# Optimization experiments

Hardware: AMD Instinct MI355X
Metric: run time of the kernel (lower is better)

## Reference

```python
import jax, jax.numpy as jnp
import numpy as np

N_NODES = 100000
N_EDGES = 1600000
IN_DIM = 64
OUT_DIM = 64
BN_EPS = 1e-5


def batchnorm(h, gamma, beta):
    # BatchNorm1d in training mode: per-feature batch stats, biased variance
    mean = jnp.mean(h, axis=0)
    var = jnp.mean((h - mean) ** 2, axis=0)
    return gamma * (h - mean) * jax.lax.rsqrt(var + BN_EPS) + beta


def setup_inputs() -> dict:
    key = jax.random.key(0)
    ks = jax.random.split(key, 4)
    x = jax.random.normal(ks[0], (N_NODES, IN_DIM), dtype=jnp.float32)
    edge_index = jax.random.randint(ks[1], (2, N_EDGES), 0, N_NODES, dtype=jnp.int32)
    epsilon = jnp.asarray(0.1, dtype=jnp.float32)
    # Linear weights stored [in, out] (transpose of torch layout)
    W1 = jax.random.normal(ks[2], (IN_DIM, 2 * OUT_DIM), dtype=jnp.float32) * (1.0 / np.sqrt(IN_DIM))
    b1 = jnp.zeros((2 * OUT_DIM,), dtype=jnp.float32)
    g1 = jnp.ones((2 * OUT_DIM,), dtype=jnp.float32)
    be1 = jnp.zeros((2 * OUT_DIM,), dtype=jnp.float32)
    W2 = jax.random.normal(ks[3], (2 * OUT_DIM, OUT_DIM), dtype=jnp.float32) * (1.0 / np.sqrt(2 * OUT_DIM))
    b2 = jnp.zeros((OUT_DIM,), dtype=jnp.float32)
    g2 = jnp.ones((OUT_DIM,), dtype=jnp.float32)
    be2 = jnp.zeros((OUT_DIM,), dtype=jnp.float32)
    return {"x": x, "edge_index": edge_index, "epsilon": epsilon,
            "W1": W1, "b1": b1, "g1": g1, "be1": be1,
            "W2": W2, "b2": b2, "g2": g2, "be2": be2}


def reference(x, edge_index, epsilon, W1, b1, g1, be1, W2, b2, g2, be2):
    src, dst = edge_index[0], edge_index[1]
    # gather messages from src, scatter-add into dst  [N, D]
    neighbor_sum = jnp.zeros_like(x).at[dst].add(x[src])
    combined = (1.0 + epsilon) * x + neighbor_sum
    h = combined @ W1 + b1            # [N, 2*out_dim]
    h = jax.nn.relu(batchnorm(h, g1, be1))
    h = h @ W2 + b2                   # [N, out_dim]
    return batchnorm(h, g2, be2)
```

## Files before the change

kernel.cpp:

```cpp
#include <hip/hip_runtime.h>

#define N_NODES 100000
#define N_EDGES 1600000
#define IN_DIM 64
#define H_DIM 128
#define OUT_DIM 64
#define BN_EPS 1e-5f
#define CAP 64
#define BIN_SHIFT 9
#define BIN_NODES 512
#define NB 256
#define NBIN_BLOCKS ((N_NODES + BIN_NODES - 1) / BIN_NODES)

#define OFF_XB     0
#define OFF_BINNED 3200000
#define OFF_COMB   3200000
#define OFF_SRCL   6400000
#define OFF_H1     6400000
#define OFF_H2     12800000
#define OFF_CNT    16000000
#define OFF_STATS  19200000
#define S1SUM 0
#define S1SQ  128
#define S2SUM 256
#define S2SQ  320

#define DEV_ATOMIC_ADD(p, v) __hip_atomic_fetch_add((p), (v), __ATOMIC_RELAXED, __HIP_MEMORY_SCOPE_AGENT)

typedef __attribute__((ext_vector_type(8))) short short8;
typedef __attribute__((ext_vector_type(4))) float f32x4;

__device__ __forceinline__ unsigned short f2bf(float f) {
  union { float f; unsigned u; } v; v.f = f;
  unsigned r = v.u + 0x7FFFu + ((v.u >> 16) & 1u);
  return (unsigned short)(r >> 16);
}
__device__ __forceinline__ float bflo(unsigned v) { union { unsigned u; float f; } t; t.u = v << 16; return t.f; }
__device__ __forceinline__ float bfhi(unsigned v) { union { unsigned u; float f; } t; t.u = v & 0xFFFF0000u; return t.f; }

__device__ __forceinline__ void acc8(float* a, uint4 v) {
  a[0] += bflo(v.x); a[1] += bfhi(v.x); a[2] += bflo(v.y); a[3] += bfhi(v.y);
  a[4] += bflo(v.z); a[5] += bfhi(v.z); a[6] += bflo(v.w); a[7] += bfhi(v.w);
}
__device__ __forceinline__ uint4 pack8(const float* a) {
  uint4 o;
  o.x = (unsigned)f2bf(a[0]) | ((unsigned)f2bf(a[1]) << 16);
  o.y = (unsigned)f2bf(a[2]) | ((unsigned)f2bf(a[3]) << 16);
  o.z = (unsigned)f2bf(a[4]) | ((unsigned)f2bf(a[5]) << 16);
  o.w = (unsigned)f2bf(a[6]) | ((unsigned)f2bf(a[7]) << 16);
  return o;
}

__global__ __launch_bounds__(256) void k_prep(const float* __restrict__ x,
                                              unsigned short* __restrict__ xb,
                                              const int* __restrict__ ei,
                                              int* __restrict__ bhist) {
  __shared__ int h[NB];
  const int tid = threadIdx.x;
  h[tid] = 0;
  #pragma unroll
  for (int j = 0; j < 8; ++j) {
    int i = blockIdx.x * 2048 + j * 256 + tid;
    if (i < N_NODES * IN_DIM / 4) {
      float4 v = ((const float4*)x)[i];
      ushort4 o;
      o.x = f2bf(v.x); o.y = f2bf(v.y); o.z = f2bf(v.z); o.w = f2bf(v.w);
      *(ushort4*)(xb + i * 4) = o;
    }
  }
  __syncthreads();
  #pragma unroll
  for (int j = 0; j < 8; ++j) {
    int e = blockIdx.x * 2048 + j * 256 + tid;
    if (e < N_EDGES) atomicAdd(&h[ei[N_EDGES + e] >> BIN_SHIFT], 1);
  }
  __syncthreads();
  if (h[tid]) DEV_ATOMIC_ADD(&bhist[tid], h[tid]);
}

__global__ __launch_bounds__(256) void k_scan256(const int* __restrict__ bhist,
                                                 int* __restrict__ boff,
                                                 int* __restrict__ bcur) {
  __shared__ int s[NB];
  const int tid = threadIdx.x;
  int v = bhist[tid];
  s[tid] = v;
  __syncthreads();
  for (int d = 1; d < NB; d <<= 1) {
    int t = (tid >= d) ? s[tid - d] : 0;
    __syncthreads();
    s[tid] += t;
    __syncthreads();
  }
  int incl = s[tid];
  boff[tid] = incl - v;
  if (tid == NB - 1) boff[NB] = incl;
  bcur[tid] = incl - v;
}

__global__ __launch_bounds__(256) void k_bsplit(const int* __restrict__ ei,
                                                int* __restrict__ bcur,
                                                int2* __restrict__ binned) {
  __shared__ int lcnt[NB];
  __shared__ int lofs[NB];
  __shared__ int lbase[NB];
  __shared__ int sc[NB];
  __shared__ int2 staged[2048];
  const int tid = threadIdx.x;
  lcnt[tid] = 0;
  __syncthreads();
  int src[8], dst[8], rk[8];
  #pragma unroll
  for (int j = 0; j < 8; ++j) {
    int e = blockIdx.x * 2048 + j * 256 + tid;
    if (e < N_EDGES) {
      src[j] = ei[e];
      dst[j] = ei[N_EDGES + e];
      rk[j] = atomicAdd(&lcnt[dst[j] >> BIN_SHIFT], 1);
    } else {
      src[j] = -1;
    }
  }
  __syncthreads();
  int v = lcnt[tid];
  sc[tid] = v;
  __syncthreads();
  for (int d = 1; d < NB; d <<= 1) {
    int t = (tid >= d) ? sc[tid - d] : 0;
    __syncthreads();
    sc[tid] += t;
    __syncthreads();
  }
  lofs[tid] = sc[tid] - v;
  if (v > 0) lbase[tid] = DEV_ATOMIC_ADD(&bcur[tid], v);
  __syncthreads();
  #pragma unroll
  for (int j = 0; j < 8; ++j) {
    if (src[j] >= 0) {
      int b = dst[j] >> BIN_SHIFT;
      staged[lofs[b] + rk[j]] = make_int2(src[j], dst[j]);
    }
  }
  int nv = sc[NB - 1];
  __syncthreads();
  for (int i = tid; i < nv; i += 256) {
    int2 e = staged[i];
    int b = e.y >> BIN_SHIFT;
    binned[lbase[b] + (i - lofs[b])] = e;
  }
}

__global__ __launch_bounds__(512) void k_bfill(const int* __restrict__ boff,
                                               const int2* __restrict__ binned,
                                               int* __restrict__ cnt,
                                               int* __restrict__ srcl) {
  __shared__ int lcnt[BIN_NODES];
  const int tid = threadIdx.x;
  for (int i = tid; i < BIN_NODES; i += 512) lcnt[i] = 0;
  __syncthreads();
  const int b = blockIdx.x;
  const int s = boff[b], e = boff[b + 1];
  const int base = b * BIN_NODES;
  for (int i = s + tid; i < e; i += 512) {
    int2 ed = binned[i];
    int pos = atomicAdd(&lcnt[ed.y - base], 1);
    if (pos < CAP) srcl[ed.y * CAP + pos] = ed.x;
  }
  __syncthreads();
  for (int i = tid; i < BIN_NODES; i += 512) {
    int node = base + i;
    if (node < N_NODES) cnt[node] = lcnt[i];
  }
}

__global__ __launch_bounds__(256, 5) void k_gather(const unsigned short* __restrict__ xb,
                                                   const float* __restrict__ eps,
                                                   const int* __restrict__ cnt,
                                                   const int* __restrict__ srcl,
                                                   unsigned short* __restrict__ comb) {
  const int t = blockIdx.x * 256 + threadIdx.x;
  const int node = t >> 3;
  const int sub = t & 7;
  if (node >= N_NODES) return;

  float a[8];
  {
    uint4 sv = *(const uint4*)(xb + node * 64 + sub * 8);
    float e1 = 1.0f + eps[0];
    a[0] = bflo(sv.x) * e1; a[1] = bfhi(sv.x) * e1;
    a[2] = bflo(sv.y) * e1; a[3] = bfhi(sv.y) * e1;
    a[4] = bflo(sv.z) * e1; a[5] = bfhi(sv.z) * e1;
    a[6] = bflo(sv.w) * e1; a[7] = bfhi(sv.w) * e1;
  }
  int deg = cnt[node];
  if (deg > CAP) deg = CAP;
  const int* sl = srcl + node * CAP;

  uint4 n0 = *(const uint4*)sl;
  uint4 n1 = *(const uint4*)(sl + 4);
  int j = 0;
  while (j + 8 <= deg) {
    uint4 i0 = n0, i1 = n1;
    uint4 r0 = *(const uint4*)(xb + (size_t)i0.x * 64 + sub * 8);
    uint4 r1 = *(const uint4*)(xb + (size_t)i0.y * 64 + sub * 8);
    uint4 r2 = *(const uint4*)(xb + (size_t)i0.z * 64 + sub * 8);
    uint4 r3 = *(const uint4*)(xb + (size_t)i0.w * 64 + sub * 8);
    uint4 r4 = *(const uint4*)(xb + (size_t)i1.x * 64 + sub * 8);
    uint4 r5 = *(const uint4*)(xb + (size_t)i1.y * 64 + sub * 8);
    uint4 r6 = *(const uint4*)(xb + (size_t)i1.z * 64 + sub * 8);
    uint4 r7 = *(const uint4*)(xb + (size_t)i1.w * 64 + sub * 8);
    j += 8;
    n0 = *(const uint4*)(sl + j);
    n1 = *(const uint4*)(sl + j + 4);
    acc8(a, r0); acc8(a, r1); acc8(a, r2); acc8(a, r3);
    acc8(a, r4); acc8(a, r5); acc8(a, r6); acc8(a, r7);
  }
  if (j + 4 <= deg) {
    uint4 i0 = *(const uint4*)(sl + j);
    uint4 r0 = *(const uint4*)(xb + (size_t)i0.x * 64 + sub * 8);
    uint4 r1 = *(const uint4*)(xb + (size_t)i0.y * 64 + sub * 8);
    uint4 r2 = *(const uint4*)(xb + (size_t)i0.z * 64 + sub * 8);
    uint4 r3 = *(const uint4*)(xb + (size_t)i0.w * 64 + sub * 8);
    acc8(a, r0); acc8(a, r1); acc8(a, r2); acc8(a, r3);
    j += 4;
  }
  if (j + 2 <= deg) {
    int2 i2 = *(const int2*)(sl + j);
    uint4 r0 = *(const uint4*)(xb + (size_t)i2.x * 64 + sub * 8);
    uint4 r1 = *(const uint4*)(xb + (size_t)i2.y * 64 + sub * 8);
    acc8(a, r0); acc8(a, r1);
    j += 2;
  }
  if (j < deg) {
    int s0 = sl[j];
    uint4 r0 = *(const uint4*)(xb + (size_t)s0 * 64 + sub * 8);
    acc8(a, r0);
  }
  *(uint4*)(comb + node * 64 + sub * 8) = pack8(a);
}

#define APAD 72
__global__ __launch_bounds__(256) void k_gemm1(const unsigned short* __restrict__ comb,
                                               const float* __restrict__ W1,
                                               const float* __restrict__ b1,
                                               unsigned short* __restrict__ h1,
                                               float* __restrict__ stats) {
  __shared__ unsigned short As[128 * APAD];
  __shared__ unsigned short Ws[128 * APAD];
  __shared__ float red[4][128];
  const int tid = threadIdx.x;
  const int wv = tid >> 6, lane = tid & 63;
  const int quad = lane >> 4, ln = lane & 15;
  const int rowBase = blockIdx.x * 128;

  #pragma unroll
  for (int it = 0; it < 8; ++it) {
    int idx = it * 256 + tid;
    int k = idx >> 5, n4 = idx & 31;
    float4 wv1 = *(const float4*)(W1 + k * 128 + n4 * 4);
    Ws[(n4 * 4 + 0) * APAD + k] = f2bf(wv1.x);
    Ws[(n4 * 4 + 1) * APAD + k] = f2bf(wv1.y);
    Ws[(n4 * 4 + 2) * APAD + k] = f2bf(wv1.z);
    Ws[(n4 * 4 + 3) * APAD + k] = f2bf(wv1.w);
  }
  #pragma unroll
  for (int it = 0; it < 4; ++it) {
    int idx = it * 256 + tid;
    int row = idx >> 3, ch = idx & 7;
    int g = rowBase * 8 + idx;
    uint4 u = (g < N_NODES * 8) ? ((const uint4*)comb)[g] : make_uint4(0, 0, 0, 0);
    *(uint4*)&As[row * APAD + ch * 8] = u;
  }
  __syncthreads();

  f32x4 acc[2][8];
  #pragma unroll
  for (int mt = 0; mt < 2; ++mt) {
    #pragma unroll
    for (int nt = 0; nt < 8; ++nt) acc[mt][nt] = (f32x4)0.0f;
  }
  const int rw = wv * 32;
  #pragma unroll
  for (int kb = 0; kb < 2; ++kb) {
    short8 a0 = *(short8*)&As[(rw + ln) * APAD + kb * 32 + quad * 8];
    short8 a1 = *(short8*)&As[(rw + 16 + ln) * APAD + kb * 32 + quad * 8];
    #pragma unroll
    for (int nt = 0; nt < 8; ++nt) {
      short8 b = *(short8*)&Ws[(nt * 16 + ln) * APAD + kb * 32 + quad * 8];
      acc[0][nt] = __builtin_amdgcn_mfma_f32_16x16x32_bf16(a0, b, acc[0][nt], 0, 0, 0);
      acc[1][nt] = __builtin_amdgcn_mfma_f32_16x16x32_bf16(a1, b, acc[1][nt], 0, 0, 0);
    }
  }

  float bias[8], s[8], q[8];
  #pragma unroll
  for (int nt = 0; nt < 8; ++nt) { bias[nt] = b1[nt * 16 + ln]; s[nt] = 0.f; q[nt] = 0.f; }
  #pragma unroll
  for (int mt = 0; mt < 2; ++mt) {
    #pragma unroll
    for (int i = 0; i < 4; ++i) {
      int gRow = rowBase + rw + mt * 16 + quad * 4 + i;
      if (gRow < N_NODES) {
        #pragma unroll
        for (int nt = 0; nt < 8; ++nt) {
          float v = acc[mt][nt][i] + bias[nt];
          h1[gRow * 128 + nt * 16 + ln] = f2bf(v);
          s[nt] += v; q[nt] += v * v;
        }
      }
    }
  }
  #pragma unroll
  for (int nt = 0; nt < 8; ++nt) {
    s[nt] += __shfl_xor(s[nt], 16); s[nt] += __shfl_xor(s[nt], 32);
    q[nt] += __shfl_xor(q[nt], 16); q[nt] += __shfl_xor(q[nt], 32);
  }
  if (lane < 16) {
    #pragma unroll
    for (int nt = 0; nt < 8; ++nt) red[wv][nt * 16 + ln] = s[nt];
  }
  __syncthreads();
  if (tid < 128) DEV_ATOMIC_ADD(&stats[S1SUM + tid],
                                red[0][tid] + red[1][tid] + red[2][tid] + red[3][tid]);
  __syncthreads();
  if (lane < 16) {
    #pragma unroll
    for (int nt = 0; nt < 8; ++nt) red[wv][nt * 16 + ln] = q[nt];
  }
  __syncthreads();
  if (tid < 128) DEV_ATOMIC_ADD(&stats[S1SQ + tid],
                                red[0][tid] + red[1][tid] + red[2][tid] + red[3][tid]);
}

#define WPAD 136
__global__ __launch_bounds__(256) void k_gemm2(const unsigned short* __restrict__ h1,
                                               const float* __restrict__ W2,
                                               const float* __restrict__ b2,
                                               const float* __restrict__ g1,
                                               const float* __restrict__ be1,
                                               unsigned short* __restrict__ h2,
                                               float* __restrict__ stats) {
  __shared__ unsigned short As[128 * APAD];
  __shared__ unsigned short Ws[64 * WPAD];
  __shared__ float red[4][64];
  __shared__ float scL[128], shL[128];
  const int tid = threadIdx.x;
  const int wv = tid >> 6, lane = tid & 63;
  const int quad = lane >> 4, ln = lane & 15;
  const int rowBase = blockIdx.x * 128;

  if (tid < 128) {
    float mean = stats[S1SUM + tid] * (1.0f / N_NODES);
    float var = stats[S1SQ + tid] * (1.0f / N_NODES) - mean * mean;
    var = fmaxf(var, 0.0f);
    float sc = g1[tid] * rsqrtf(var + BN_EPS);
    scL[tid] = sc;
    shL[tid] = be1[tid] - mean * sc;
  }
  #pragma unroll
  for (int it = 0; it < 8; ++it) {
    int idx = it * 256 + tid;
    int k = idx >> 4, n4 = idx & 15;
    float4 wv2 = *(const float4*)(W2 + k * 64 + n4 * 4);
    Ws[(n4 * 4 + 0) * WPAD + k] = f2bf(wv2.x);
    Ws[(n4 * 4 + 1) * WPAD + k] = f2bf(wv2.y);
    Ws[(n4 * 4 + 2) * WPAD + k] = f2bf(wv2.z);
    Ws[(n4 * 4 + 3) * WPAD + k] = f2bf(wv2.w);
  }

  f32x4 acc[2][4];
  #pragma unroll
  for (int mt = 0; mt < 2; ++mt) {
    #pragma unroll
    for (int nt = 0; nt < 4; ++nt) acc[mt][nt] = (f32x4)0.0f;
  }
  const int rw = wv * 32;

  for (int kc = 0; kc < 2; ++kc) {
    __syncthreads();
    #pragma unroll
    for (int it = 0; it < 4; ++it) {
      int idx = it * 256 + tid;
      int row = idx >> 3, ch = idx & 7;
      int gRow = rowBase + row;
      uint4 u = (gRow < N_NODES) ? *(const uint4*)(h1 + gRow * 128 + kc * 64 + ch * 8)
                                 : make_uint4(0, 0, 0, 0);
      int kb = kc * 64 + ch * 8;
      float f0 = fmaxf(bflo(u.x) * scL[kb + 0] + shL[kb + 0], 0.f);
      float f1 = fmaxf(bfhi(u.x) * scL[kb + 1] + shL[kb + 1], 0.f);
      float f2 = fmaxf(bflo(u.y) * scL[kb + 2] + shL[kb + 2], 0.f);
      float f3 = fmaxf(bfhi(u.y) * scL[kb + 3] + shL[kb + 3], 0.f);
      float f4 = fmaxf(bflo(u.z) * scL[kb + 4] + shL[kb + 4], 0.f);
      float f5 = fmaxf(bfhi(u.z) * scL[kb + 5] + shL[kb + 5], 0.f);
      float f6 = fmaxf(bflo(u.w) * scL[kb + 6] + shL[kb + 6], 0.f);
      float f7 = fmaxf(bfhi(u.w) * scL[kb + 7] + shL[kb + 7], 0.f);
      uint4 o;
      o.x = (unsigned)f2bf(f0) | ((unsigned)f2bf(f1) << 16);
      o.y = (unsigned)f2bf(f2) | ((unsigned)f2bf(f3) << 16);
      o.z = (unsigned)f2bf(f4) | ((unsigned)f2bf(f5) << 16);
      o.w = (unsigned)f2bf(f6) | ((unsigned)f2bf(f7) << 16);
      *(uint4*)&As[row * APAD + ch * 8] = o;
    }
    __syncthreads();
    #pragma unroll
    for (int kb = 0; kb < 2; ++kb) {
      short8 a0 = *(short8*)&As[(rw + ln) * APAD + kb * 32 + quad * 8];
      short8 a1 = *(short8*)&As[(rw + 16 + ln) * APAD + kb * 32 + quad * 8];
      #pragma unroll
      for (int nt = 0; nt < 4; ++nt) {
        short8 b = *(short8*)&Ws[(nt * 16 + ln) * WPAD + kc * 64 + kb * 32 + quad * 8];
        acc[0][nt] = __builtin_amdgcn_mfma_f32_16x16x32_bf16(a0, b, acc[0][nt], 0, 0, 0);
        acc[1][nt] = __builtin_amdgcn_mfma_f32_16x16x32_bf16(a1, b, acc[1][nt], 0, 0, 0);
      }
    }
  }

  float bias[4], s[4], q[4];
  #pragma unroll
  for (int nt = 0; nt < 4; ++nt) { bias[nt] = b2[nt * 16 + ln]; s[nt] = 0.f; q[nt] = 0.f; }
  #pragma unroll
  for (int mt = 0; mt < 2; ++mt) {
    #pragma unroll
    for (int i = 0; i < 4; ++i) {
      int gRow = rowBase + rw + mt * 16 + quad * 4 + i;
      if (gRow < N_NODES) {
        #pragma unroll
        for (int nt = 0; nt < 4; ++nt) {
          float v = acc[mt][nt][i] + bias[nt];
          h2[gRow * 64 + nt * 16 + ln] = f2bf(v);
          s[nt] += v; q[nt] += v * v;
        }
      }
    }
  }
  #pragma unroll
  for (int nt = 0; nt < 4; ++nt) {
    s[nt] += __shfl_xor(s[nt], 16); s[nt] += __shfl_xor(s[nt], 32);
    q[nt] += __shfl_xor(q[nt], 16); q[nt] += __shfl_xor(q[nt], 32);
  }
  if (lane < 16) {
    #pragma unroll
    for (int nt = 0; nt < 4; ++nt) red[wv][nt * 16 + ln] = s[nt];
  }
  __syncthreads();
  if (tid < 64) DEV_ATOMIC_ADD(&stats[S2SUM + tid],
                               red[0][tid] + red[1][tid] + red[2][tid] + red[3][tid]);
  __syncthreads();
  if (lane < 16) {
    #pragma unroll
    for (int nt = 0; nt < 4; ++nt) red[wv][nt * 16 + ln] = q[nt];
  }
  __syncthreads();
  if (tid < 64) DEV_ATOMIC_ADD(&stats[S2SQ + tid],
                               red[0][tid] + red[1][tid] + red[2][tid] + red[3][tid]);
}

__global__ __launch_bounds__(256) void k_out(const unsigned short* __restrict__ h2,
                                             const float* __restrict__ stats,
                                             const float* __restrict__ g2,
                                             const float* __restrict__ be2,
                                             float* __restrict__ out) {
  __shared__ float scL[64], shL[64];
  const int tid = threadIdx.x;
  if (tid < 64) {
    float mean = stats[S2SUM + tid] * (1.0f / N_NODES);
    float var = stats[S2SQ + tid] * (1.0f / N_NODES) - mean * mean;
    var = fmaxf(var, 0.0f);
    float sc = g2[tid] * rsqrtf(var + BN_EPS);
    scL[tid] = sc;
    shL[tid] = be2[tid] - mean * sc;
  }
  __syncthreads();
  int i = blockIdx.x * 256 + tid;
  if (i < N_NODES * OUT_DIM / 4) {
    int c = i & 15;
    uint2 u = *(const uint2*)(h2 + i * 4);
    float4 v = {bflo(u.x), bfhi(u.x), bflo(u.y), bfhi(u.y)};
    float4 sc = ((const float4*)scL)[c];
    float4 sh = ((const float4*)shL)[c];
    v.x = v.x * sc.x + sh.x;
    v.y = v.y * sc.y + sh.y;
    v.z = v.z * sc.z + sh.z;
    v.w = v.w * sc.w + sh.w;
    ((float4*)out)[i] = v;
  }
}

extern "C" void kernel_launch(void* const* d_in, const int* in_sizes, int n_in,
                              void* d_out, int out_size, void* d_ws, size_t ws_size,
                              hipStream_t stream) {
  const float* x   = (const float*)d_in[0];
  const int*   ei  = (const int*)d_in[1];
  const float* eps = (const float*)d_in[2];
  const float* W1  = (const float*)d_in[3];
  const float* b1  = (const float*)d_in[4];
  const float* g1  = (const float*)d_in[5];
  const float* be1 = (const float*)d_in[6];
  const float* W2  = (const float*)d_in[7];
  const float* b2  = (const float*)d_in[8];
  const float* g2  = (const float*)d_in[9];
  const float* be2 = (const float*)d_in[10];

  float* ws = (float*)d_ws;
  unsigned short* xb     = (unsigned short*)(ws + OFF_XB);
  int2*           binned = (int2*)(ws + OFF_BINNED);
  unsigned short* comb   = (unsigned short*)(ws + OFF_COMB);
  int*            srcl   = (int*)(ws + OFF_SRCL);
  unsigned short* h1     = (unsigned short*)(ws + OFF_H1);
  unsigned short* h2     = (unsigned short*)(ws + OFF_H2);
  int*            cnt    = (int*)(ws + OFF_CNT);
  float*          stats  = ws + OFF_STATS;
  int*            bhist  = (int*)(stats + 768);
  int*            boff   = (int*)(stats + 1024);
  int*            bcur   = (int*)(stats + 1288);
  float*          out    = (float*)d_out;

  hipMemsetAsync(stats, 0, 1024 * sizeof(float), stream);

  const int edgeGrid = (N_EDGES + 2047) / 2048;
  const int gemmGrid = (N_NODES + 127) / 128;
  const int gatherGrid = (N_NODES * 8 + 255) / 256;
  k_prep<<<edgeGrid, 256, 0, stream>>>(x, xb, ei, bhist);
  k_scan256<<<1, NB, 0, stream>>>(bhist, boff, bcur);
  k_bsplit<<<edgeGrid, 256, 0, stream>>>(ei, bcur, binned);
  k_bfill<<<NBIN_BLOCKS, 512, 0, stream>>>(boff, binned, cnt, srcl);
  k_gather<<<gatherGrid, 256, 0, stream>>>(xb, eps, cnt, srcl, comb);
  k_gemm1<<<gemmGrid, 256, 0, stream>>>(comb, W1, b1, h1, stats);
  k_gemm2<<<gemmGrid, 256, 0, stream>>>(h1, W2, b2, g1, be1, h2, stats);
  k_out<<<(N_NODES * OUT_DIM / 4 + 255) / 256, 256, 0, stream>>>(h2, stats, g2, be2, out);
}
```

Baseline: 257.8 us.

## Fuse both GEMMs, batchnorms and output into one kernel with grid barriers

```diff
diff --git a/kernel.cpp b/kernel.cpp
--- a/kernel.cpp
+++ b/kernel.cpp
@@ -11,13 +11,12 @@
 #define BIN_NODES 512
 #define NB 256
 #define NBIN_BLOCKS ((N_NODES + BIN_NODES - 1) / BIN_NODES)
+#define MLP_GRID ((N_NODES + 127) / 128)
 
 #define OFF_XB     0
 #define OFF_BINNED 3200000
 #define OFF_COMB   3200000
 #define OFF_SRCL   6400000
-#define OFF_H1     6400000
-#define OFF_H2     12800000
 #define OFF_CNT    16000000
 #define OFF_STATS  19200000
 #define S1SUM 0
@@ -239,29 +238,53 @@
   *(uint4*)(comb + node * 64 + sub * 8) = pack8(a);
 }
 
-#define APAD 72
-__global__ __launch_bounds__(256) void k_gemm1(const unsigned short* __restrict__ comb,
-                                               const float* __restrict__ W1,
-                                               const float* __restrict__ b1,
-                                               unsigned short* __restrict__ h1,
-                                               float* __restrict__ stats) {
-  __shared__ unsigned short As[128 * APAD];
-  __shared__ unsigned short Ws[128 * APAD];
+#define KP 68
+#define HP 136
+
+__device__ __forceinline__ void gridbar(int* bar, int nblk) {
+  __syncthreads();
+  if (threadIdx.x == 0) {
+    __hip_atomic_fetch_add(bar, 1, __ATOMIC_ACQ_REL, __HIP_MEMORY_SCOPE_AGENT);
+    while (__hip_atomic_load(bar, __ATOMIC_ACQUIRE, __HIP_MEMORY_SCOPE_AGENT) < nblk) {
+      __builtin_amdgcn_s_sleep(4);
+    }
+  }
+  __syncthreads();
+}
+
+__global__ __launch_bounds__(256, 4) void k_mlp(const unsigned short* __restrict__ comb,
+                                                const float* __restrict__ W1,
+                                                const float* __restrict__ b1,
+                                                const float* __restrict__ g1,
+                                                const float* __restrict__ be1,
+                                                const float* __restrict__ W2,
+                                                const float* __restrict__ b2,
+                                                const float* __restrict__ g2,
+                                                const float* __restrict__ be2,
+                                                float* __restrict__ stats,
+                                                int* __restrict__ bar,
+                                                float* __restrict__ out) {
+  __shared__ unsigned short smem[17408];
   __shared__ float red[4][128];
+  __shared__ float scl[128], shl[128];
+  unsigned short* As  = smem;
+  unsigned short* Ws1 = smem + 128 * KP;
+  unsigned short* H   = smem;
   const int tid = threadIdx.x;
   const int wv = tid >> 6, lane = tid & 63;
   const int quad = lane >> 4, ln = lane & 15;
   const int rowBase = blockIdx.x * 128;
+  const int nblk = gridDim.x;
 
   #pragma unroll
   for (int it = 0; it < 8; ++it) {
     int idx = it * 256 + tid;
     int k = idx >> 5, n4 = idx & 31;
     float4 wv1 = *(const float4*)(W1 + k * 128 + n4 * 4);
-    Ws[(n4 * 4 + 0) * APAD + k] = f2bf(wv1.x);
-    Ws[(n4 * 4 + 1) * APAD + k] = f2bf(wv1.y);
-    Ws[(n4 * 4 + 2) * APAD + k] = f2bf(wv1.z);
-    Ws[(n4 * 4 + 3) * APAD + k] = f2bf(wv1.w);
+    Ws1[(n4 * 4 + 0) * KP + k] = f2bf(wv1.x);
+    Ws1[(n4 * 4 + 1) * KP + k] = f2bf(wv1.y);
+    Ws1[(n4 * 4 + 2) * KP + k] = f2bf(wv1.z);
+    Ws1[(n4 * 4 + 3) * KP + k] = f2bf(wv1.w);
   }
   #pragma unroll
   for (int it = 0; it < 4; ++it) {
@@ -269,155 +292,197 @@
     int row = idx >> 3, ch = idx & 7;
     int g = rowBase * 8 + idx;
     uint4 u = (g < N_NODES * 8) ? ((const uint4*)comb)[g] : make_uint4(0, 0, 0, 0);
-    *(uint4*)&As[row * APAD + ch * 8] = u;
+    *(uint4*)&As[row * KP + ch * 8] = u;
   }
   __syncthreads();
 
   f32x4 acc[2][8];
   #pragma unroll
-  for (int mt = 0; mt < 2; ++mt) {
+  for (int mt = 0; mt < 2; ++mt)
     #pragma unroll
     for (int nt = 0; nt < 8; ++nt) acc[mt][nt] = (f32x4)0.0f;
-  }
   const int rw = wv * 32;
   #pragma unroll
   for (int kb = 0; kb < 2; ++kb) {
-    short8 a0 = *(short8*)&As[(rw + ln) * APAD + kb * 32 + quad * 8];
-    short8 a1 = *(short8*)&As[(rw + 16 + ln) * APAD + kb * 32 + quad * 8];
+    short8 a0 = *(short8*)&As[(rw + ln) * KP + kb * 32 + quad * 8];
+    short8 a1 = *(short8*)&As[(rw + 16 + ln) * KP + kb * 32 + quad * 8];
     #pragma unroll
     for (int nt = 0; nt < 8; ++nt) {
-      short8 b = *(short8*)&Ws[(nt * 16 + ln) * APAD + kb * 32 + quad * 8];
+      short8 b = *(short8*)&Ws1[(nt * 16 + ln) * KP + kb * 32 + quad * 8];
       acc[0][nt] = __builtin_amdgcn_mfma_f32_16x16x32_bf16(a0, b, acc[0][nt], 0, 0, 0);
       acc[1][nt] = __builtin_amdgcn_mfma_f32_16x16x32_bf16(a1, b, acc[1][nt], 0, 0, 0);
     }
   }
-
-  float bias[8], s[8], q[8];
-  #pragma unroll
-  for (int nt = 0; nt < 8; ++nt) { bias[nt] = b1[nt * 16 + ln]; s[nt] = 0.f; q[nt] = 0.f; }
-  #pragma unroll
-  for (int mt = 0; mt < 2; ++mt) {
-    #pragma unroll
-    for (int i = 0; i < 4; ++i) {
-      int gRow = rowBase + rw + mt * 16 + quad * 4 + i;
-      if (gRow < N_NODES) {
+  __syncthreads();
+
+  {
+    float bias[8], s[8], q[8];
+    #pragma unroll
+    for (int nt = 0; nt < 8; ++nt) { bias[nt] = b1[nt * 16 + ln]; s[nt] = 0.f; q[nt] = 0.f; }
+    #pragma unroll
+    for (int mt = 0; mt < 2; ++mt) {
+      #pragma unroll
+      for (int i = 0; i < 4; ++i) {
+        int lRow = rw + mt * 16 + quad * 4 + i;
+        int gRow = rowBase + lRow;
+        bool ok = gRow < N_NODES;
         #pragma unroll
         for (int nt = 0; nt < 8; ++nt) {
           float v = acc[mt][nt][i] + bias[nt];
-          h1[gRow * 128 + nt * 16 + ln] = f2bf(v);
-          s[nt] += v; q[nt] += v * v;
+          H[lRow * HP + nt * 16 + ln] = f2bf(v);
+          if (ok) { s[nt] += v; q[nt] += v * v; }
         }
       }
     }
-  }
-  #pragma unroll
-  for (int nt = 0; nt < 8; ++nt) {
-    s[nt] += __shfl_xor(s[nt], 16); s[nt] += __shfl_xor(s[nt], 32);
-    q[nt] += __shfl_xor(q[nt], 16); q[nt] += __shfl_xor(q[nt], 32);
-  }
-  if (lane < 16) {
-    #pragma unroll
-    for (int nt = 0; nt < 8; ++nt) red[wv][nt * 16 + ln] = s[nt];
-  }
-  __syncthreads();
-  if (tid < 128) DEV_ATOMIC_ADD(&stats[S1SUM + tid],
-                                red[0][tid] + red[1][tid] + red[2][tid] + red[3][tid]);
-  __syncthreads();
-  if (lane < 16) {
-    #pragma unroll
-    for (int nt = 0; nt < 8; ++nt) red[wv][nt * 16 + ln] = q[nt];
-  }
-  __syncthreads();
-  if (tid < 128) DEV_ATOMIC_ADD(&stats[S1SQ + tid],
-                                red[0][tid] + red[1][tid] + red[2][tid] + red[3][tid]);
-}
-
-#define WPAD 136
-__global__ __launch_bounds__(256) void k_gemm2(const unsigned short* __restrict__ h1,
-                                               const float* __restrict__ W2,
-                                               const float* __restrict__ b2,
-                                               const float* __restrict__ g1,
-                                               const float* __restrict__ be1,
-                                               unsigned short* __restrict__ h2,
-                                               float* __restrict__ stats) {
-  __shared__ unsigned short As[128 * APAD];
-  __shared__ unsigned short Ws[64 * WPAD];
-  __shared__ float red[4][64];
-  __shared__ float scL[128], shL[128];
-  const int tid = threadIdx.x;
-  const int wv = tid >> 6, lane = tid & 63;
-  const int quad = lane >> 4, ln = lane & 15;
-  const int rowBase = blockIdx.x * 128;
+    #pragma unroll
+    for (int nt = 0; nt < 8; ++nt) {
+      s[nt] += __shfl_xor(s[nt], 16); s[nt] += __shfl_xor(s[nt], 32);
+      q[nt] += __shfl_xor(q[nt], 16); q[nt] += __shfl_xor(q[nt], 32);
+    }
+    if (lane < 16) {
+      #pragma unroll
+      for (int nt = 0; nt < 8; ++nt) red[wv][nt * 16 + ln] = s[nt];
+    }
+    __syncthreads();
+    if (tid < 128) DEV_ATOMIC_ADD(&stats[S1SUM + tid],
+                                  red[0][tid] + red[1][tid] + red[2][tid] + red[3][tid]);
+    __syncthreads();
+    if (lane < 16) {
+      #pragma unroll
+      for (int nt = 0; nt < 8; ++nt) red[wv][nt * 16 + ln] = q[nt];
+    }
+    __syncthreads();
+    if (tid < 128) DEV_ATOMIC_ADD(&stats[S1SQ + tid],
+                                  red[0][tid] + red[1][tid] + red[2][tid] + red[3][tid]);
+  }
+
+  gridbar(&bar[0], nblk);
 
   if (tid < 128) {
-    float mean = stats[S1SUM + tid] * (1.0f / N_NODES);
-    float var = stats[S1SQ + tid] * (1.0f / N_NODES) - mean * mean;
+    float su = __hip_atomic_load(&stats[S1SUM + tid], __ATOMIC_ACQUIRE, __HIP_MEMORY_SCOPE_AGENT);
+    float sq = __hip_atomic_load(&stats[S1SQ + tid], __ATOMIC_ACQUIRE, __HIP_MEMORY_SCOPE_AGENT);
+    float mean = su * (1.0f / N_NODES);
+    float var = sq * (1.0f / N_NODES) - mean * mean;
     var = fmaxf(var, 0.0f);
     float sc = g1[tid] * rsqrtf(var + BN_EPS);
-    scL[tid] = sc;
-    shL[tid] = be1[tid] - mean * sc;
-  }
+    scl[tid] = sc;
+    shl[tid] = be1[tid] - mean * sc;
+  }
+  __syncthreads();
+
   #pragma unroll
   for (int it = 0; it < 8; ++it) {
     int idx = it * 256 + tid;
-    int k = idx >> 4, n4 = idx & 15;
-    float4 wv2 = *(const float4*)(W2 + k * 64 + n4 * 4);
-    Ws[(n4 * 4 + 0) * WPAD + k] = f2bf(wv2.x);
-    Ws[(n4 * 4 + 1) * WPAD + k] = f2bf(wv2.y);
-    Ws[(n4 * 4 + 2) * WPAD + k] = f2bf(wv2.z);
-    Ws[(n4 * 4 + 3) * WPAD + k] = f2bf(wv2.w);
-  }
-
-  f32x4 acc[2][4];
-  #pragma unroll
-  for (int mt = 0; mt < 2; ++mt) {
-    #pragma unroll
-    for (int nt = 0; nt < 4; ++nt) acc[mt][nt] = (f32x4)0.0f;
-  }
-  const int rw = wv * 32;
-
+    int row = idx >> 4, ch = idx & 15;
+    uint4* p = (uint4*)&H[row * HP + ch * 8];
+    uint4 u = *p;
+    int kb = ch * 8;
+    float f0 = fmaxf(bflo(u.x) * scl[kb + 0] + shl[kb + 0], 0.f);
+    float f1 = fmaxf(bfhi(u.x) * scl[kb + 1] + shl[kb + 1], 0.f);
+    float f2 = fmaxf(bflo(u.y) * scl[kb + 2] + shl[kb + 2], 0.f);
+    float f3 = fmaxf(bfhi(u.y) * scl[kb + 3] + shl[kb + 3], 0.f);
+    float f4 = fmaxf(bflo(u.z) * scl[kb + 4] + shl[kb + 4], 0.f);
+    float f5 = fmaxf(bfhi(u.z) * scl[kb + 5] + shl[kb + 5], 0.f);
+    float f6 = fmaxf(bflo(u.w) * scl[kb + 6] + shl[kb + 6], 0.f);
+    float f7 = fmaxf(bfhi(u.w) * scl[kb + 7] + shl[kb + 7], 0.f);
+    uint4 o;
+    o.x = (unsigned)f2bf(f0) | ((unsigned)f2bf(f1) << 16);
+    o.y = (unsigned)f2bf(f2) | ((unsigned)f2bf(f3) << 16);
+    o.z = (unsigned)f2bf(f4) | ((unsigned)f2bf(f5) << 16);
+    o.w = (unsigned)f2bf(f6) | ((unsigned)f2bf(f7) << 16);
+    *p = o;
+  }
+  __syncthreads();
+
+  f32x4 acc2[2][4];
+  #pragma unroll
+  for (int mt = 0; mt < 2; ++mt)
+    #pragma unroll
+    for (int nt = 0; nt < 4; ++nt) acc2[mt][nt] = (f32x4)0.0f;
+
+  #pragma unroll
   for (int kc = 0; kc < 2; ++kc) {
-    __syncthreads();
-    #pragma unroll
-    for (int it = 0; it < 4; ++it) {
-      int idx = it * 256 + tid;
-      int row = idx >> 3, ch = idx & 7;
-      int gRow = rowBase + row;
-      uint4 u = (gRow < N_NODES) ? *(const uint4*)(h1 + gRow * 128 + kc * 64 + ch * 8)
-                                 : make_uint4(0, 0, 0, 0);
-      int kb = kc * 64 + ch * 8;
-      float f0 = fmaxf(bflo(u.x) * scL[kb + 0] + shL[kb + 0], 0.f);
-      float f1 = fmaxf(bfhi(u.x) * scL[kb + 1] + shL[kb + 1], 0.f);
-      float f2 = fmaxf(bflo(u.y) * scL[kb + 2] + shL[kb + 2], 0.f);
-      float f3 = fmaxf(bfhi(u.y) * scL[kb + 3] + shL[kb + 3], 0.f);
-      float f4 = fmaxf(bflo(u.z) * scL[kb + 4] + shL[kb + 4], 0.f);
-      float f5 = fmaxf(bfhi(u.z) * scL[kb + 5] + shL[kb + 5], 0.f);
-      float f6 = fmaxf(bflo(u.w) * scL[kb + 6] + shL[kb + 6], 0.f);
-      float f7 = fmaxf(bfhi(u.w) * scL[kb + 7] + shL[kb + 7], 0.f);
-      uint4 o;
-      o.x = (unsigned)f2bf(f0) | ((unsigned)f2bf(f1) << 16);
-      o.y = (unsigned)f2bf(f2) | ((unsigned)f2bf(f3) << 16);
-      o.z = (unsigned)f2bf(f4) | ((unsigned)f2bf(f5) << 16);
-      o.w = (unsigned)f2bf(f6) | ((unsigned)f2bf(f7) << 16);
-      *(uint4*)&As[row * APAD + ch * 8] = o;
-    }
-    __syncthreads();
+    short8 wf[4][2];
+    #pragma unroll
+    for (int nt = 0; nt < 4; ++nt) {
+      #pragma unroll
+      for (int kb = 0; kb < 2; ++kb) {
+        short8 f;
+        #pragma unroll
+        for (int j = 0; j < 8; ++j) {
+          int k = kc * 64 + kb * 32 + quad * 8 + j;
+          f[j] = (short)f2bf(W2[k * 64 + nt * 16 + ln]);
+        }
+        wf[nt][kb] = f;
+      }
+    }
     #pragma unroll
     for (int kb = 0; kb < 2; ++kb) {
-      short8 a0 = *(short8*)&As[(rw + ln) * APAD + kb * 32 + quad * 8];
-      short8 a1 = *(short8*)&As[(rw + 16 + ln) * APAD + kb * 32 + quad * 8];
+      short8 a0 = *(short8*)&H[(rw + ln) * HP + kc * 64 + kb * 32 + quad * 8];
+      short8 a1 = *(short8*)&H[(rw + 16 + ln) * HP + kc * 64 + kb * 32 + quad * 8];
       #pragma unroll
       for (int nt = 0; nt < 4; ++nt) {
-        short8 b = *(short8*)&Ws[(nt * 16 + ln) * WPAD + kc * 64 + kb * 32 + quad * 8];
-        acc[0][nt] = __builtin_amdgcn_mfma_f32_16x16x32_bf16(a0, b, acc[0][nt], 0, 0, 0);
-        acc[1][nt] = __builtin_amdgcn_mfma_f32_16x16x32_bf16(a1, b, acc[1][nt], 0, 0, 0);
+        acc2[0][nt] = __builtin_amdgcn_mfma_f32_16x16x32_bf16(a0, wf[nt][kb], acc2[0][nt], 0, 0, 0);
+        acc2[1][nt] = __builtin_amdgcn_mfma_f32_16x16x32_bf16(a1, wf[nt][kb], acc2[1][nt], 0, 0, 0);
       }
     }
   }
 
-  float bias[4], s[4], q[4];
-  #pragma unroll
-  for (int nt = 0; nt < 4; ++nt) { bias[nt] = b2[nt * 16 + ln]; s[nt] = 0.f; q[nt] = 0.f; }
+  {
+    float bias[4], s[4], q[4];
+    #pragma unroll
+    for (int nt = 0; nt < 4; ++nt) { bias[nt] = b2[nt * 16 + ln]; s[nt] = 0.f; q[nt] = 0.f; }
+    #pragma unroll
+    for (int mt = 0; mt < 2; ++mt) {
+      #pragma unroll
+      for (int i = 0; i < 4; ++i) {
+        int gRow = rowBase + rw + mt * 16 + quad * 4 + i;
+        bool ok = gRow < N_NODES;
+        #pragma unroll
+        for (int nt = 0; nt < 4; ++nt) {
+          float v = acc2[mt][nt][i] + bias[nt];
+          if (ok) { s[nt] += v; q[nt] += v * v; }
+          acc2[mt][nt][i] = bflo((unsigned)f2bf(v));
+        }
+      }
+    }
+    #pragma unroll
+    for (int nt = 0; nt < 4; ++nt) {
+      s[nt] += __shfl_xor(s[nt], 16); s[nt] += __shfl_xor(s[nt], 32);
+      q[nt] += __shfl_xor(q[nt], 16); q[nt] += __shfl_xor(q[nt], 32);
+    }
+    if (lane < 16) {
+      #pragma unroll
+      for (int nt = 0; nt < 4; ++nt) red[wv][nt * 16 + ln] = s[nt];
+    }
+    __syncthreads();
+    if (tid < 64) DEV_ATOMIC_ADD(&stats[S2SUM + tid],
+                                 red[0][tid] + red[1][tid] + red[2][tid] + red[3][tid]);
+    __syncthreads();
+    if (lane < 16) {
+      #pragma unroll
+      for (int nt = 0; nt < 4; ++nt) red[wv][nt * 16 + ln] = q[nt];
+    }
+    __syncthreads();
+    if (tid < 64) DEV_ATOMIC_ADD(&stats[S2SQ + tid],
+                                 red[0][tid] + red[1][tid] + red[2][tid] + red[3][tid]);
+  }
+
+  gridbar(&bar[1], nblk);
+
+  float sc2[4], sh2[4];
+  #pragma unroll
+  for (int nt = 0; nt < 4; ++nt) {
+    int c = nt * 16 + ln;
+    float su = __hip_atomic_load(&stats[S2SUM + c], __ATOMIC_ACQUIRE, __HIP_MEMORY_SCOPE_AGENT);
+    float sq = __hip_atomic_load(&stats[S2SQ + c], __ATOMIC_ACQUIRE, __HIP_MEMORY_SCOPE_AGENT);
+    float mean = su * (1.0f / N_NODES);
+    float var = sq * (1.0f / N_NODES) - mean * mean;
+    var = fmaxf(var, 0.0f);
+    float sc = g2[c] * rsqrtf(var + BN_EPS);
+    sc2[nt] = sc;
+    sh2[nt] = be2[c] - mean * sc;
+  }
   #pragma unroll
   for (int mt = 0; mt < 2; ++mt) {
     #pragma unroll
@@ -426,63 +491,10 @@
       if (gRow < N_NODES) {
         #pragma unroll
         for (int nt = 0; nt < 4; ++nt) {
-          float v = acc[mt][nt][i] + bias[nt];
-          h2[gRow * 64 + nt * 16 + ln] = f2bf(v);
-          s[nt] += v; q[nt] += v * v;
+          out[gRow * 64 + nt * 16 + ln] = acc2[mt][nt][i] * sc2[nt] + sh2[nt];
         }
       }
     }
-  }
-  #pragma unroll
-  for (int nt = 0; nt < 4; ++nt) {
-    s[nt] += __shfl_xor(s[nt], 16); s[nt] += __shfl_xor(s[nt], 32);
-    q[nt] += __shfl_xor(q[nt], 16); q[nt] += __shfl_xor(q[nt], 32);
-  }
-  if (lane < 16) {
-    #pragma unroll
-    for (int nt = 0; nt < 4; ++nt) red[wv][nt * 16 + ln] = s[nt];
-  }
-  __syncthreads();
-  if (tid < 64) DEV_ATOMIC_ADD(&stats[S2SUM + tid],
-                               red[0][tid] + red[1][tid] + red[2][tid] + red[3][tid]);
-  __syncthreads();
-  if (lane < 16) {
-    #pragma unroll
-    for (int nt = 0; nt < 4; ++nt) red[wv][nt * 16 + ln] = q[nt];
-  }
-  __syncthreads();
-  if (tid < 64) DEV_ATOMIC_ADD(&stats[S2SQ + tid],
-                               red[0][tid] + red[1][tid] + red[2][tid] + red[3][tid]);
-}
-
-__global__ __launch_bounds__(256) void k_out(const unsigned short* __restrict__ h2,
-                                             const float* __restrict__ stats,
-                                             const float* __restrict__ g2,
-                                             const float* __restrict__ be2,
-                                             float* __restrict__ out) {
-  __shared__ float scL[64], shL[64];
-  const int tid = threadIdx.x;
-  if (tid < 64) {
-    float mean = stats[S2SUM + tid] * (1.0f / N_NODES);
-    float var = stats[S2SQ + tid] * (1.0f / N_NODES) - mean * mean;
-    var = fmaxf(var, 0.0f);
-    float sc = g2[tid] * rsqrtf(var + BN_EPS);
-    scL[tid] = sc;
-    shL[tid] = be2[tid] - mean * sc;
-  }
-  __syncthreads();
-  int i = blockIdx.x * 256 + tid;
-  if (i < N_NODES * OUT_DIM / 4) {
-    int c = i & 15;
-    uint2 u = *(const uint2*)(h2 + i * 4);
-    float4 v = {bflo(u.x), bfhi(u.x), bflo(u.y), bfhi(u.y)};
-    float4 sc = ((const float4*)scL)[c];
-    float4 sh = ((const float4*)shL)[c];
-    v.x = v.x * sc.x + sh.x;
-    v.y = v.y * sc.y + sh.y;
-    v.z = v.z * sc.z + sh.z;
-    v.w = v.w * sc.w + sh.w;
-    ((float4*)out)[i] = v;
   }
 }
 
@@ -506,26 +518,23 @@
   int2*           binned = (int2*)(ws + OFF_BINNED);
   unsigned short* comb   = (unsigned short*)(ws + OFF_COMB);
   int*            srcl   = (int*)(ws + OFF_SRCL);
-  unsigned short* h1     = (unsigned short*)(ws + OFF_H1);
-  unsigned short* h2     = (unsigned short*)(ws + OFF_H2);
   int*            cnt    = (int*)(ws + OFF_CNT);
   float*          stats  = ws + OFF_STATS;
   int*            bhist  = (int*)(stats + 768);
   int*            boff   = (int*)(stats + 1024);
   int*            bcur   = (int*)(stats + 1288);
+  int*            bar    = (int*)(stats + 1544);
   float*          out    = (float*)d_out;
 
-  hipMemsetAsync(stats, 0, 1024 * sizeof(float), stream);
+  hipMemsetAsync(stats, 0, 1552 * sizeof(float), stream);
 
   const int edgeGrid = (N_EDGES + 2047) / 2048;
-  const int gemmGrid = (N_NODES + 127) / 128;
   const int gatherGrid = (N_NODES * 8 + 255) / 256;
   k_prep<<<edgeGrid, 256, 0, stream>>>(x, xb, ei, bhist);
   k_scan256<<<1, NB, 0, stream>>>(bhist, boff, bcur);
   k_bsplit<<<edgeGrid, 256, 0, stream>>>(ei, bcur, binned);
   k_bfill<<<NBIN_BLOCKS, 512, 0, stream>>>(boff, binned, cnt, srcl);
   k_gather<<<gatherGrid, 256, 0, stream>>>(xb, eps, cnt, srcl, comb);
-  k_gemm1<<<gemmGrid, 256, 0, stream>>>(comb, W1, b1, h1, stats);
-  k_gemm2<<<gemmGrid, 256, 0, stream>>>(h1, W2, b2, g1, be1, h2, stats);
-  k_out<<<(N_NODES * OUT_DIM / 4 + 255) / 256, 256, 0, stream>>>(h2, stats, g2, be2, out);
-}
+  k_mlp<<<MLP_GRID, 256, 0, stream>>>(comb, W1, b1, g1, be1, W2, b2, g2, be2,
+                                      stats, bar, out);
+}
```

Result: slower. 586.2 us (+127.4%).

## Replace histogram-scan edge binning with fixed-capacity per-bin buckets

Applied to the files above, without the earlier changes.

```diff
diff --git a/kernel.cpp b/kernel.cpp
--- a/kernel.cpp
+++ b/kernel.cpp
@@ -10,16 +10,17 @@
 #define BIN_SHIFT 9
 #define BIN_NODES 512
 #define NB 256
+#define BINCAP 10240
 #define NBIN_BLOCKS ((N_NODES + BIN_NODES - 1) / BIN_NODES)
 
 #define OFF_XB     0
-#define OFF_BINNED 3200000
-#define OFF_COMB   3200000
-#define OFF_SRCL   6400000
-#define OFF_H1     6400000
-#define OFF_H2     12800000
-#define OFF_CNT    16000000
-#define OFF_STATS  19200000
+#define OFF_SRCL   3200000
+#define OFF_BINNED 9600000
+#define OFF_COMB   15000000
+#define OFF_H1     18200000
+#define OFF_H2     24600000
+#define OFF_CNT    27800000
+#define OFF_STATS  28000000
 #define S1SUM 0
 #define S1SQ  128
 #define S2SUM 256
@@ -51,13 +52,15 @@
   return o;
 }
 
-__global__ __launch_bounds__(256) void k_prep(const float* __restrict__ x,
-                                              unsigned short* __restrict__ xb,
-                                              const int* __restrict__ ei,
-                                              int* __restrict__ bhist) {
-  __shared__ int h[NB];
+__global__ __launch_bounds__(256) void k_bsplit(const float* __restrict__ x,
+                                                unsigned short* __restrict__ xb,
+                                                const int* __restrict__ ei,
+                                                int* __restrict__ bcnt,
+                                                int2* __restrict__ binned) {
+  __shared__ int lcnt[NB];
+  __shared__ int lbase[NB];
   const int tid = threadIdx.x;
-  h[tid] = 0;
+  lcnt[tid] = 0;
   #pragma unroll
   for (int j = 0; j < 8; ++j) {
     int i = blockIdx.x * 2048 + j * 256 + tid;
@@ -68,46 +71,6 @@
       *(ushort4*)(xb + i * 4) = o;
     }
   }
-  __syncthreads();
-  #pragma unroll
-  for (int j = 0; j < 8; ++j) {
-    int e = blockIdx.x * 2048 + j * 256 + tid;
-    if (e < N_EDGES) atomicAdd(&h[ei[N_EDGES + e] >> BIN_SHIFT], 1);
-  }
-  __syncthreads();
-  if (h[tid]) DEV_ATOMIC_ADD(&bhist[tid], h[tid]);
-}
-
-__global__ __launch_bounds__(256) void k_scan256(const int* __restrict__ bhist,
-                                                 int* __restrict__ boff,
-                                                 int* __restrict__ bcur) {
-  __shared__ int s[NB];
-  const int tid = threadIdx.x;
-  int v = bhist[tid];
-  s[tid] = v;
-  __syncthreads();
-  for (int d = 1; d < NB; d <<= 1) {
-    int t = (tid >= d) ? s[tid - d] : 0;
-    __syncthreads();
-    s[tid] += t;
-    __syncthreads();
-  }
-  int incl = s[tid];
-  boff[tid] = incl - v;
-  if (tid == NB - 1) boff[NB] = incl;
-  bcur[tid] = incl - v;
-}
-
-__global__ __launch_bounds__(256) void k_bsplit(const int* __restrict__ ei,
-                                                int* __restrict__ bcur,
-                                                int2* __restrict__ binned) {
-  __shared__ int lcnt[NB];
-  __shared__ int lofs[NB];
-  __shared__ int lbase[NB];
-  __shared__ int sc[NB];
-  __shared__ int2 staged[2048];
-  const int tid = threadIdx.x;
-  lcnt[tid] = 0;
   __syncthreads();
   int src[8], dst[8], rk[8];
   #pragma unroll
@@ -122,35 +85,19 @@
     }
   }
   __syncthreads();
-  int v = lcnt[tid];
-  sc[tid] = v;
-  __syncthreads();
-  for (int d = 1; d < NB; d <<= 1) {
-    int t = (tid >= d) ? sc[tid - d] : 0;
-    __syncthreads();
-    sc[tid] += t;
-    __syncthreads();
-  }
-  lofs[tid] = sc[tid] - v;
-  if (v > 0) lbase[tid] = DEV_ATOMIC_ADD(&bcur[tid], v);
+  if (lcnt[tid] > 0) lbase[tid] = DEV_ATOMIC_ADD(&bcnt[tid], lcnt[tid]);
   __syncthreads();
   #pragma unroll
   for (int j = 0; j < 8; ++j) {
     if (src[j] >= 0) {
       int b = dst[j] >> BIN_SHIFT;
-      staged[lofs[b] + rk[j]] = make_int2(src[j], dst[j]);
-    }
-  }
-  int nv = sc[NB - 1];
-  __syncthreads();
-  for (int i = tid; i < nv; i += 256) {
-    int2 e = staged[i];
-    int b = e.y >> BIN_SHIFT;
-    binned[lbase[b] + (i - lofs[b])] = e;
-  }
-}
-
-__global__ __launch_bounds__(512) void k_bfill(const int* __restrict__ boff,
+      int pos = lbase[b] + rk[j];
+      if (pos < BINCAP) binned[b * BINCAP + pos] = make_int2(src[j], dst[j]);
+    }
+  }
+}
+
+__global__ __launch_bounds__(512) void k_bfill(const int* __restrict__ bcnt,
                                                const int2* __restrict__ binned,
                                                int* __restrict__ cnt,
                                                int* __restrict__ srcl) {
@@ -159,10 +106,12 @@
   for (int i = tid; i < BIN_NODES; i += 512) lcnt[i] = 0;
   __syncthreads();
   const int b = blockIdx.x;
-  const int s = boff[b], e = boff[b + 1];
+  int n = bcnt[b];
+  if (n > BINCAP) n = BINCAP;
+  const int2* run = binned + b * BINCAP;
   const int base = b * BIN_NODES;
-  for (int i = s + tid; i < e; i += 512) {
-    int2 ed = binned[i];
+  for (int i = tid; i < n; i += 512) {
+    int2 ed = run[i];
     int pos = atomicAdd(&lcnt[ed.y - base], 1);
     if (pos < CAP) srcl[ed.y * CAP + pos] = ed.x;
   }
@@ -503,16 +452,14 @@
 
   float* ws = (float*)d_ws;
   unsigned short* xb     = (unsigned short*)(ws + OFF_XB);
+  int*            srcl   = (int*)(ws + OFF_SRCL);
   int2*           binned = (int2*)(ws + OFF_BINNED);
   unsigned short* comb   = (unsigned short*)(ws + OFF_COMB);
-  int*            srcl   = (int*)(ws + OFF_SRCL);
   unsigned short* h1     = (unsigned short*)(ws + OFF_H1);
   unsigned short* h2     = (unsigned short*)(ws + OFF_H2);
   int*            cnt    = (int*)(ws + OFF_CNT);
   float*          stats  = ws + OFF_STATS;
-  int*            bhist  = (int*)(stats + 768);
-  int*            boff   = (int*)(stats + 1024);
-  int*            bcur   = (int*)(stats + 1288);
+  int*            bcnt   = (int*)(stats + 768);
   float*          out    = (float*)d_out;
 
   hipMemsetAsync(stats, 0, 1024 * sizeof(float), stream);
@@ -520,10 +467,8 @@
   const int edgeGrid = (N_EDGES + 2047) / 2048;
   const int gemmGrid = (N_NODES + 127) / 128;
   const int gatherGrid = (N_NODES * 8 + 255) / 256;
-  k_prep<<<edgeGrid, 256, 0, stream>>>(x, xb, ei, bhist);
-  k_scan256<<<1, NB, 0, stream>>>(bhist, boff, bcur);
-  k_bsplit<<<edgeGrid, 256, 0, stream>>>(ei, bcur, binned);
-  k_bfill<<<NBIN_BLOCKS, 512, 0, stream>>>(boff, binned, cnt, srcl);
+  k_bsplit<<<edgeGrid, 256, 0, stream>>>(x, xb, ei, bcnt, binned);
+  k_bfill<<<NBIN_BLOCKS, 512, 0, stream>>>(bcnt, binned, cnt, srcl);
   k_gather<<<gatherGrid, 256, 0, stream>>>(xb, eps, cnt, srcl, comb);
   k_gemm1<<<gemmGrid, 256, 0, stream>>>(comb, W1, b1, h1, stats);
   k_gemm2<<<gemmGrid, 256, 0, stream>>>(h1, W2, b2, g1, be1, h2, stats);
```

Result: faster. 239.2 us (-7.2%).
